# Kernel tuning notes

Hardware: AMD Instinct MI355X
Metric: run time of the kernel (lower is better)

The kernel has to match this reference:

```python
import jax, jax.numpy as jnp
import numpy as np

B, S, H, L = 16, 512, 768, 4096

def setup_inputs() -> dict:
    key = jax.random.key(0)
    k1, k2, k3 = jax.random.split(key, 3)
    inputs = jax.random.normal(k1, (B, S, H), dtype=jnp.float32)
    # realistic variable-length masks: each sequence has length in [S//2, S]
    lengths = jax.random.randint(k2, (B,), S // 2, S + 1)
    masks = jnp.arange(S)[None, :] < lengths[:, None]  # [B, S] bool
    # xavier_uniform for Linear(H, L, bias=False): weight shape [L, H]
    limit = float(np.sqrt(6.0 / (H + L)))
    W = jax.random.uniform(k3, (L, H), minval=-limit, maxval=limit, dtype=jnp.float32)
    return {"inputs": inputs, "masks": masks, "W": W}

def reference(inputs, masks, W):
    # scores: Linear(inputs) -> [B,S,L], transposed to [B,L,S]
    scores = jnp.einsum("bsh,lh->bls", inputs, W)
    scores = jnp.where(masks[:, None, :], scores, -jnp.inf)
    attn = jax.nn.softmax(scores, axis=-1)  # over seq dim
    # weighted sum pooling: [B,L,S] @ [B,S,H] -> [B,L,H]
    return jnp.einsum("bls,bsh->blh", attn, inputs)
```

## Files before the change

kernel.cpp:

```cpp
#include <hip/hip_runtime.h>
#include <hip/hip_bf16.h>

#define Bn 16
#define Sn 512
#define Hn 768
#define Ln 4096

typedef __attribute__((ext_vector_type(8))) short bf16x8;
typedef __attribute__((ext_vector_type(4))) float f32x4;

using bf16 = __hip_bfloat16;

constexpr int BL = 64;

constexpr int SM_BYTES  = 75776;
constexpr int PH2_BUF   = 36864;
constexpr int WS_OFF_IN = 32768;
constexpr int P_OFF     = 0;
constexpr int REDM_OFF  = 73728;
constexpr int REDS_OFF  = 74752;

typedef const __attribute__((address_space(1))) unsigned int* gas_ptr;
typedef __attribute__((address_space(3))) unsigned int* las_ptr;

__device__ __forceinline__ void gld_lds16(const void* g, void* l) {
  __builtin_amdgcn_global_load_lds((gas_ptr)g, (las_ptr)l, 16, 0, 0);
}

__device__ __forceinline__ unsigned short bfbits(float x) {
  __hip_bfloat16 h = __float2bfloat16(x);
  unsigned short u;
  __builtin_memcpy(&u, &h, 2);
  return u;
}

union Pack8 { bf16 h[8]; uint4 u; };

__device__ inline uint4 cvt8(float4 a, float4 b) {
  Pack8 p;
  p.h[0] = __float2bfloat16(a.x); p.h[1] = __float2bfloat16(a.y);
  p.h[2] = __float2bfloat16(a.z); p.h[3] = __float2bfloat16(a.w);
  p.h[4] = __float2bfloat16(b.x); p.h[5] = __float2bfloat16(b.y);
  p.h[6] = __float2bfloat16(b.z); p.h[7] = __float2bfloat16(b.w);
  return p.u;
}

__global__ __launch_bounds__(256) void convert_x_kernel(
    const float* __restrict__ X, bf16* __restrict__ Xbf, bf16* __restrict__ XT) {
  __shared__ bf16 t[64][72];
  const int tid = threadIdx.x;
  const int b  = blockIdx.z;
  const int s0 = blockIdx.y * 64;
  const int h0 = blockIdx.x * 64;
  const int r = tid >> 2;
  const int p = tid & 3;
  const float* src = X + ((size_t)b * Sn + s0 + r) * Hn + h0 + p * 16;
  float4 a0 = *(const float4*)(src + 0);
  float4 a1 = *(const float4*)(src + 4);
  float4 a2 = *(const float4*)(src + 8);
  float4 a3 = *(const float4*)(src + 12);
  uint4 u0 = cvt8(a0, a1);
  uint4 u1 = cvt8(a2, a3);
  bf16* xb = Xbf + ((size_t)b * Sn + s0 + r) * Hn + h0 + p * 16;
  *(uint4*)(xb)     = u0;
  *(uint4*)(xb + 8) = u1;
  *(uint4*)&t[r][p * 16]     = u0;
  *(uint4*)&t[r][p * 16 + 8] = u1;
  __syncthreads();
  Pack8 o0, o1;
#pragma unroll
  for (int i = 0; i < 8; ++i) {
    o0.h[i] = t[p * 16 + i][r];
    o1.h[i] = t[p * 16 + 8 + i][r];
  }
  bf16* xt = XT + ((size_t)b * Hn + h0 + r) * Sn + s0 + p * 16;
  *(uint4*)(xt)     = o0.u;
  *(uint4*)(xt + 8) = o1.u;
}

__global__ __launch_bounds__(256) void convert_w_kernel(
    const float* __restrict__ W, bf16* __restrict__ Wbf) {
  const size_t i = ((size_t)blockIdx.x * 256 + threadIdx.x) * 8;
  float4 a0 = *(const float4*)(W + i);
  float4 a1 = *(const float4*)(W + i + 4);
  *(uint4*)(Wbf + i) = cvt8(a0, a1);
}

__global__ __launch_bounds__(256, 2) void attn_main_kernel(
    const int* __restrict__ masks,
    const bf16* __restrict__ Xbf, const bf16* __restrict__ XTg,
    const bf16* __restrict__ Wbf, float* __restrict__ out) {
  __shared__ char sm[SM_BYTES];
  const int tid  = threadIdx.x;
  const int w    = tid >> 6;
  const int lane = tid & 63;
  const int col  = lane & 15;
  const int quad = lane >> 4;
  const int lg   = w >> 1;
  const int sg   = w & 1;
  const int vb = (blockIdx.x & 7) * 128 + (blockIdx.x >> 3);
  const int b  = vb >> 6;
  const int l0 = (vb & 63) * BL;

  float bias_r[8];
  {
    const int* mrow = masks + b * Sn + w * 128 + col;
#pragma unroll
    for (int nt = 0; nt < 8; ++nt)
      bias_r[nt] = mrow[nt * 16] ? 0.0f : -1e30f;
  }

  const f32x4 zero = {0.f, 0.f, 0.f, 0.f};
  f32x4 acc[4][8];
#pragma unroll
  for (int am = 0; am < 4; ++am)
#pragma unroll
    for (int nt = 0; nt < 8; ++nt) acc[am][nt] = zero;

  const int rr2 = lane >> 2;
  const int cc2 = (lane & 3) * 8;

#define STAGE2(BUFOFF, K0)                                                         \
  {                                                                                \
    const bf16* gx = Xbf + ((size_t)b * Sn + w * 128 + rr2) * Hn + (K0) + cc2;     \
    char* dx = sm + (BUFOFF) + (w * 128) * 64;                                     \
    _Pragma("unroll")                                                              \
    for (int i = 0; i < 8; ++i) {                                                  \
      gld_lds16(gx, dx);                                                           \
      gx += 16 * Hn;                                                               \
      dx += 16 * 64;                                                               \
    }                                                                              \
    const bf16* gw = Wbf + ((size_t)(l0 + w * 16 + rr2)) * Hn + (K0) + cc2;        \
    gld_lds16(gw, sm + (BUFOFF) + WS_OFF_IN + (w * 16) * 64);                      \
  }

#define PH2_COMPUTE(BUFOFF)                                                        \
  {                                                                                \
    const char* xs = sm + (BUFOFF);                                                \
    const char* ws = sm + (BUFOFF) + WS_OFF_IN;                                    \
    bf16x8 aF[4], bF[8];                                                           \
    _Pragma("unroll")                                                              \
    for (int am = 0; am < 4; ++am)                                                 \
      aF[am] = *(const bf16x8*)&ws[(am * 16 + col) * 64 + quad * 16];              \
    _Pragma("unroll")                                                              \
    for (int nt = 0; nt < 8; ++nt)                                                 \
      bF[nt] = *(const bf16x8*)&xs[(w * 128 + nt * 16 + col) * 64 + quad * 16];    \
    _Pragma("unroll")                                                              \
    for (int nt = 0; nt < 8; ++nt)                                                 \
      _Pragma("unroll")                                                            \
      for (int am = 0; am < 4; ++am)                                               \
        acc[am][nt] = __builtin_amdgcn_mfma_f32_16x16x32_bf16(aF[am], bF[nt], acc[am][nt], 0, 0, 0); \
  }

  STAGE2(0, 0);
  asm volatile("s_waitcnt vmcnt(0)" ::: "memory");
  __builtin_amdgcn_s_barrier();
  for (int k0 = 0; k0 < Hn; k0 += 64) {
    STAGE2(PH2_BUF, k0 + 32);
    PH2_COMPUTE(0);
    asm volatile("s_waitcnt vmcnt(0)" ::: "memory");
    __builtin_amdgcn_s_barrier();
    if (k0 + 64 < Hn) STAGE2(0, k0 + 64);
    PH2_COMPUTE(PH2_BUF);
    asm volatile("s_waitcnt vmcnt(0)" ::: "memory");
    __builtin_amdgcn_s_barrier();
  }
#undef STAGE2
#undef PH2_COMPUTE

  float* redm = (float*)&sm[REDM_OFF];
  float* reds = (float*)&sm[REDS_OFF];
  float mx[4][4];
#pragma unroll
  for (int am = 0; am < 4; ++am)
#pragma unroll
    for (int r = 0; r < 4; ++r) mx[am][r] = -3e38f;
#pragma unroll
  for (int am = 0; am < 4; ++am)
#pragma unroll
    for (int nt = 0; nt < 8; ++nt)
#pragma unroll
      for (int r = 0; r < 4; ++r) {
        acc[am][nt][r] += bias_r[nt];
        mx[am][r] = fmaxf(mx[am][r], acc[am][nt][r]);
      }
#pragma unroll
  for (int am = 0; am < 4; ++am)
#pragma unroll
    for (int r = 0; r < 4; ++r) {
      mx[am][r] = fmaxf(mx[am][r], __shfl_xor(mx[am][r], 1, 64));
      mx[am][r] = fmaxf(mx[am][r], __shfl_xor(mx[am][r], 2, 64));
      mx[am][r] = fmaxf(mx[am][r], __shfl_xor(mx[am][r], 4, 64));
      mx[am][r] = fmaxf(mx[am][r], __shfl_xor(mx[am][r], 8, 64));
    }
  if (col == 0) {
#pragma unroll
    for (int am = 0; am < 4; ++am)
#pragma unroll
      for (int r = 0; r < 4; ++r)
        redm[w * 64 + am * 16 + quad * 4 + r] = mx[am][r];
  }
  __syncthreads();
  float gmax[4][4], sum[4][4];
#pragma unroll
  for (int am = 0; am < 4; ++am)
#pragma unroll
    for (int r = 0; r < 4; ++r) {
      const int row = am * 16 + quad * 4 + r;
      gmax[am][r] = fmaxf(fmaxf(redm[row], redm[64 + row]),
                          fmaxf(redm[128 + row], redm[192 + row]));
      sum[am][r] = 0.f;
    }
#pragma unroll
  for (int am = 0; am < 4; ++am)
#pragma unroll
    for (int nt = 0; nt < 8; ++nt)
#pragma unroll
      for (int r = 0; r < 4; ++r) {
        const float e = __expf(acc[am][nt][r] - gmax[am][r]);
        acc[am][nt][r] = e;
        sum[am][r] += e;
      }
#pragma unroll
  for (int am = 0; am < 4; ++am)
#pragma unroll
    for (int r = 0; r < 4; ++r) {
      sum[am][r] += __shfl_xor(sum[am][r], 1, 64);
      sum[am][r] += __shfl_xor(sum[am][r], 2, 64);
      sum[am][r] += __shfl_xor(sum[am][r], 4, 64);
      sum[am][r] += __shfl_xor(sum[am][r], 8, 64);
    }
  if (col == 0) {
#pragma unroll
    for (int am = 0; am < 4; ++am)
#pragma unroll
      for (int r = 0; r < 4; ++r)
        reds[w * 64 + am * 16 + quad * 4 + r] = sum[am][r];
  }
  __syncthreads();
  float rs[4][4];
#pragma unroll
  for (int am = 0; am < 4; ++am)
#pragma unroll
    for (int r = 0; r < 4; ++r) {
      const int row = am * 16 + quad * 4 + r;
      rs[am][r] = 1.0f / (reds[row] + reds[64 + row] + reds[128 + row] + reds[192 + row]);
    }

  const int pi = col & 1;
#pragma unroll
  for (int am = 0; am < 4; ++am)
#pragma unroll
    for (int t = 0; t < 4; ++t)
#pragma unroll
      for (int r = 0; r < 4; ++r) {
        const float own0 = acc[am][2 * t][r];
        const float own1 = acc[am][2 * t + 1][r];
        const float p0 = __shfl_xor(own0, 1, 64);
        const float p1 = __shfl_xor(own1, 1, 64);
        const float lo = pi ? p1 : own0;
        const float hi = pi ? own1 : p0;
        const unsigned pk = (unsigned)bfbits(lo) | ((unsigned)bfbits(hi) << 16);
        const int nt_w = 2 * t + pi;
        const int row = am * 16 + quad * 4 + r;
        const int sp = w * 128 + nt_w * 16 + (col & ~1);
        const int slot = (sp >> 3) ^ (row & 7);
        *(unsigned*)&sm[P_OFF + row * 1024 + slot * 16 + (sp & 7) * 2] = pk;
      }

  __syncthreads();

  bf16x8 preg[2][16];
#pragma unroll
  for (int a = 0; a < 2; ++a) {
    const int row = lg * 32 + a * 16 + col;
#pragma unroll
    for (int kf = 0; kf < 16; ++kf) {
      const int slot = (kf * 4 + quad) ^ (row & 7);
      preg[a][kf] = *(const bf16x8*)&sm[P_OFF + row * 1024 + slot * 16];
    }
  }
  __syncthreads();

  const int rr5 = lane >> 3;
  const int cc5 = lane & 7;
  auto stage_xt = [&](int bufoff, int n0, int s0) {
    const int r0 = w * 32;
    const bf16* g = XTg + ((size_t)b * Hn + n0 * 128 + r0 + rr5) * Sn + s0 + (cc5 ^ rr5) * 8;
#pragma unroll
    for (int i = 0; i < 4; ++i) {
      gld_lds16(g, &sm[bufoff + (r0 + i * 8) * 128]);
      g += 8 * Sn;
    }
  };

  stage_xt(0, 0, 0);
  asm volatile("s_waitcnt vmcnt(0)" ::: "memory");
  __builtin_amdgcn_s_barrier();

  for (int n0 = 0; n0 < Hn / 128; ++n0) {
    f32x4 oacc[2][4];
#pragma unroll
    for (int a = 0; a < 2; ++a)
#pragma unroll
      for (int nt = 0; nt < 4; ++nt) oacc[a][nt] = zero;
#pragma unroll
    for (int s0i = 0; s0i < 8; ++s0i) {
      const int par = s0i & 1;
      if (s0i < 7)           stage_xt((par ^ 1) * 16384, n0, (s0i + 1) * 64);
      else if (n0 < Hn / 128 - 1) stage_xt((par ^ 1) * 16384, n0 + 1, 0);
#pragma unroll
      for (int ks = 0; ks < 2; ++ks) {
        const int kf = s0i * 2 + ks;
        const bf16x8 pa0 = preg[0][kf];
        const bf16x8 pa1 = preg[1][kf];
#pragma unroll
        for (int nt = 0; nt < 4; ++nt) {
          const int hl = (nt * 2 + sg) * 16 + col;
          const int xslot = (ks * 4 + quad) ^ (hl & 7);
          bf16x8 xb = *(const bf16x8*)&sm[par * 16384 + hl * 128 + xslot * 16];
          oacc[0][nt] = __builtin_amdgcn_mfma_f32_16x16x32_bf16(pa0, xb, oacc[0][nt], 0, 0, 0);
          oacc[1][nt] = __builtin_amdgcn_mfma_f32_16x16x32_bf16(pa1, xb, oacc[1][nt], 0, 0, 0);
        }
      }
      asm volatile("s_waitcnt vmcnt(0)" ::: "memory");
      __builtin_amdgcn_s_barrier();
    }
#pragma unroll
    for (int a = 0; a < 2; ++a)
#pragma unroll
      for (int nt = 0; nt < 4; ++nt) {
        const int h = n0 * 128 + (nt * 2 + sg) * 16 + col;
        const int lbase = l0 + lg * 32 + a * 16 + quad * 4;
#pragma unroll
        for (int r = 0; r < 4; ++r)
          out[((size_t)b * Ln + lbase + r) * Hn + h] = oacc[a][nt][r] * rs[lg * 2 + a][r];
      }
  }
}

__global__ __launch_bounds__(256) void attn_fallback_kernel(
    const float* __restrict__ X, const int* __restrict__ masks,
    const float* __restrict__ W, float* __restrict__ out) {
  __shared__ float sc[4][Sn];
  const int wv = threadIdx.x >> 6, lane = threadIdx.x & 63;
  const int gw = blockIdx.x * 4 + wv;
  const int b = gw / Ln, l = gw % Ln;
  float wreg[12];
#pragma unroll
  for (int j = 0; j < 12; ++j) wreg[j] = W[(size_t)l * Hn + j * 64 + lane];
  for (int s = 0; s < Sn; ++s) {
    const float* xr = X + ((size_t)b * Sn + s) * Hn;
    float p = 0.f;
#pragma unroll
    for (int j = 0; j < 12; ++j) p += xr[j * 64 + lane] * wreg[j];
#pragma unroll
    for (int off = 32; off > 0; off >>= 1) p += __shfl_xor(p, off, 64);
    if (lane == 0) sc[wv][s] = p;
  }
  __syncthreads();
  float m = -3e38f;
#pragma unroll
  for (int i = 0; i < 8; ++i) {
    const int s = lane * 8 + i;
    const float v = sc[wv][s] + (masks[b * Sn + s] ? 0.f : -1e30f);
    sc[wv][s] = v;
    m = fmaxf(m, v);
  }
#pragma unroll
  for (int off = 32; off > 0; off >>= 1) m = fmaxf(m, __shfl_xor(m, off, 64));
  __syncthreads();
  float sum = 0.f;
#pragma unroll
  for (int i = 0; i < 8; ++i) {
    const int s = lane * 8 + i;
    const float e = __expf(sc[wv][s] - m);
    sc[wv][s] = e;
    sum += e;
  }
#pragma unroll
  for (int off = 32; off > 0; off >>= 1) sum += __shfl_xor(sum, off, 64);
  const float rs = 1.0f / sum;
  __syncthreads();
  float o[12];
#pragma unroll
  for (int j = 0; j < 12; ++j) o[j] = 0.f;
  for (int s = 0; s < Sn; ++s) {
    const float p = sc[wv][s];
    const float* xr = X + ((size_t)b * Sn + s) * Hn;
#pragma unroll
    for (int j = 0; j < 12; ++j) o[j] += p * xr[j * 64 + lane];
  }
#pragma unroll
  for (int j = 0; j < 12; ++j)
    out[((size_t)b * Ln + l) * Hn + j * 64 + lane] = o[j] * rs;
}

extern "C" void kernel_launch(void* const* d_in, const int* in_sizes, int n_in,
                              void* d_out, int out_size, void* d_ws, size_t ws_size,
                              hipStream_t stream) {
  const float* X     = (const float*)d_in[0];
  const int*   masks = (const int*)d_in[1];
  const float* W     = (const float*)d_in[2];
  float* out = (float*)d_out;

  const size_t need = ((size_t)2 * Bn * Sn * Hn + (size_t)Ln * Hn) * sizeof(bf16);
  if (ws_size >= need) {
    bf16* Xbf = (bf16*)d_ws;
    bf16* XT  = Xbf + (size_t)Bn * Sn * Hn;
    bf16* Wbf = XT  + (size_t)Bn * Sn * Hn;
    convert_x_kernel<<<dim3(Hn / 64, Sn / 64, Bn), 256, 0, stream>>>(X, Xbf, XT);
    convert_w_kernel<<<dim3((Ln * Hn) / 2048), 256, 0, stream>>>(W, Wbf);
    attn_main_kernel<<<dim3(Bn * (Ln / BL)), 256, 0, stream>>>(masks, Xbf, XT, Wbf, out);
  } else {
    attn_fallback_kernel<<<dim3(Bn * Ln / 4), 256, 0, stream>>>(X, masks, W, out);
  }
}
```

Measured before the change: 359.3 us.

## Load W fragments directly to registers and drop barriers in score GEMM loop

The score-GEMM main loop no longer stages W tiles through LDS. Each wave loads its MFMA A fragments for W straight from global memory into a double-buffered register array. The X tile is still staged to LDS, but each wave reads only its own 128-row slice, so the block-wide barriers are replaced by per-wave vmcnt waits with two stages in flight. This shrinks the LDS footprint and removes the cross-wave barrier stalls, at the cost of more VGPRs and uncoalesced 16-byte global loads of W.

```diff
diff --git a/kernel.cpp b/kernel.cpp
--- a/kernel.cpp
+++ b/kernel.cpp
@@ -13,12 +13,10 @@
 
 constexpr int BL = 64;
 
-constexpr int SM_BYTES  = 75776;
-constexpr int PH2_BUF   = 36864;
-constexpr int WS_OFF_IN = 32768;
+constexpr int SM_BYTES  = 67584;
 constexpr int P_OFF     = 0;
-constexpr int REDM_OFF  = 73728;
-constexpr int REDS_OFF  = 74752;
+constexpr int REDM_OFF  = 65536;
+constexpr int REDS_OFF  = 66560;
 
 typedef const __attribute__((address_space(1))) unsigned int* gas_ptr;
 typedef __attribute__((address_space(3))) unsigned int* las_ptr;
@@ -117,56 +115,62 @@
 #pragma unroll
     for (int nt = 0; nt < 8; ++nt) acc[am][nt] = zero;
 
-  const int rr2 = lane >> 2;
-  const int cc2 = (lane & 3) * 8;
-
-#define STAGE2(BUFOFF, K0)                                                         \
-  {                                                                                \
-    const bf16* gx = Xbf + ((size_t)b * Sn + w * 128 + rr2) * Hn + (K0) + cc2;     \
-    char* dx = sm + (BUFOFF) + (w * 128) * 64;                                     \
-    _Pragma("unroll")                                                              \
-    for (int i = 0; i < 8; ++i) {                                                  \
-      gld_lds16(gx, dx);                                                           \
-      gx += 16 * Hn;                                                               \
-      dx += 16 * 64;                                                               \
-    }                                                                              \
-    const bf16* gw = Wbf + ((size_t)(l0 + w * 16 + rr2)) * Hn + (K0) + cc2;        \
-    gld_lds16(gw, sm + (BUFOFF) + WS_OFF_IN + (w * 16) * 64);                      \
-  }
-
-#define PH2_COMPUTE(BUFOFF)                                                        \
-  {                                                                                \
-    const char* xs = sm + (BUFOFF);                                                \
-    const char* ws = sm + (BUFOFF) + WS_OFF_IN;                                    \
-    bf16x8 aF[4], bF[8];                                                           \
-    _Pragma("unroll")                                                              \
-    for (int am = 0; am < 4; ++am)                                                 \
-      aF[am] = *(const bf16x8*)&ws[(am * 16 + col) * 64 + quad * 16];              \
-    _Pragma("unroll")                                                              \
-    for (int nt = 0; nt < 8; ++nt)                                                 \
-      bF[nt] = *(const bf16x8*)&xs[(w * 128 + nt * 16 + col) * 64 + quad * 16];    \
-    _Pragma("unroll")                                                              \
-    for (int nt = 0; nt < 8; ++nt)                                                 \
-      _Pragma("unroll")                                                            \
-      for (int am = 0; am < 4; ++am)                                               \
-        acc[am][nt] = __builtin_amdgcn_mfma_f32_16x16x32_bf16(aF[am], bF[nt], acc[am][nt], 0, 0, 0); \
-  }
-
-  STAGE2(0, 0);
-  asm volatile("s_waitcnt vmcnt(0)" ::: "memory");
-  __builtin_amdgcn_s_barrier();
-  for (int k0 = 0; k0 < Hn; k0 += 64) {
-    STAGE2(PH2_BUF, k0 + 32);
-    PH2_COMPUTE(0);
-    asm volatile("s_waitcnt vmcnt(0)" ::: "memory");
-    __builtin_amdgcn_s_barrier();
-    if (k0 + 64 < Hn) STAGE2(0, k0 + 64);
-    PH2_COMPUTE(PH2_BUF);
-    asm volatile("s_waitcnt vmcnt(0)" ::: "memory");
-    __builtin_amdgcn_s_barrier();
-  }
-#undef STAGE2
-#undef PH2_COMPUTE
+  {
+    const int rr2 = lane >> 2;
+    const int cc2 = (lane & 3) * 8;
+    const bf16* xsrc = Xbf + ((size_t)b * Sn + w * 128 + rr2) * Hn + cc2;
+    const bf16* wbase = Wbf + ((size_t)(l0 + col)) * Hn + quad * 8;
+
+    bf16x8 aFbuf[2][4];
+
+#define LOAD_AF(P, N)                                                            \
+    {                                                                            \
+      _Pragma("unroll")                                                          \
+      for (int am = 0; am < 4; ++am)                                             \
+        aFbuf[P][am] = *(const bf16x8*)(wbase + (size_t)am * 16 * Hn + (N) * 32); \
+    }
+
+#define STAGE_XS(P, N)                                                           \
+    {                                                                            \
+      const bf16* g = xsrc + (N) * 32;                                           \
+      char* d = sm + (P) * 32768 + (w * 128) * 64;                               \
+      _Pragma("unroll")                                                          \
+      for (int i = 0; i < 8; ++i) {                                              \
+        gld_lds16(g, d);                                                         \
+        g += 16 * Hn;                                                            \
+        d += 1024;                                                               \
+      }                                                                          \
+    }
+
+    LOAD_AF(0, 0); STAGE_XS(0, 0);
+    LOAD_AF(1, 1); STAGE_XS(1, 1);
+
+#pragma unroll
+    for (int n = 0; n < 24; ++n) {
+      const int p = n & 1;
+      if (n < 23) {
+        asm volatile("s_waitcnt vmcnt(12)" ::: "memory");
+      } else {
+        asm volatile("s_waitcnt vmcnt(0)" ::: "memory");
+      }
+      bf16x8 bF[8];
+#pragma unroll
+      for (int nt = 0; nt < 8; ++nt)
+        bF[nt] = *(const bf16x8*)&sm[p * 32768 + (w * 128 + nt * 16 + col) * 64 + quad * 16];
+      asm volatile("s_waitcnt lgkmcnt(0)" ::: "memory");
+#pragma unroll
+      for (int nt = 0; nt < 8; ++nt)
+#pragma unroll
+        for (int am = 0; am < 4; ++am)
+          acc[am][nt] = __builtin_amdgcn_mfma_f32_16x16x32_bf16(aFbuf[p][am], bF[nt], acc[am][nt], 0, 0, 0);
+      if (n < 22) {
+        LOAD_AF(p, n + 2);
+        STAGE_XS(p, n + 2);
+      }
+    }
+#undef LOAD_AF
+#undef STAGE_XS
+  }
 
   float* redm = (float*)&sm[REDM_OFF];
   float* reds = (float*)&sm[REDS_OFF];
```

Measured after the change: 367.4 us. +2.3%, slower.
